# Kernel optimization log

Measured on AMD Instinct MI355X. Metric: run time of the kernel, lower is better.

Reference implementation:

```python
import jax, jax.numpy as jnp
import numpy as np

INITIAL_DELTA = 0.1
DELTA_LOW = 0.02
DELTA_HIGH = 0.1
SCAN_LEN_OFFSET = 20  # scan over num_columns - 20
EXTRA_LO, EXTRA_HI = 232, 252  # pass-through columns


def setup_inputs() -> dict:
    key = jax.random.key(0)
    x = jax.random.normal(key, (128, 1024, 252), dtype=jnp.float32)
    return {"x": x}


def _delta_modulate(x):
    # x: [B, R, C]; scan over first C-20 columns with per-(b,r) state.
    B, R, C = x.shape
    n_steps = C - SCAN_LEN_OFFSET
    xs = jnp.moveaxis(x[:, :, :n_steps], -1, 0)  # [n_steps, B, R]

    dc0 = jnp.zeros((B, R), dtype=x.dtype)
    delta0 = jnp.full((B, R), INITIAL_DELTA, dtype=x.dtype)
    tc0 = jnp.zeros((B, R), dtype=x.dtype)
    ntc0 = jnp.zeros((B, R), dtype=x.dtype)

    def step(carry, x_i):
        dc, delta, tc, ntc = carry
        up = x_i > (dc + delta)
        dn = x_i < (dc - delta)
        trig = up | dn
        tc = jnp.where(trig, tc + 1.0, 0.0)
        ntc = jnp.where(trig, 0.0, ntc + 1.0)
        delta = jnp.where(tc >= 3.0, DELTA_LOW, delta)
        delta = jnp.where(ntc >= 3.0, DELTA_HIGH, delta)
        dc = jnp.where(trig, x_i, dc)
        return (dc, delta, tc, ntc), (up, dn)

    _, (UP, DN) = jax.lax.scan(step, (dc0, delta0, tc0, ntc0), xs)
    # UP/DN: [n_steps, B, R] bool -> [B, R, n_steps]
    UP = jnp.moveaxis(UP, 0, -1)
    DN = jnp.moveaxis(DN, 0, -1)
    encoded = jnp.concatenate([UP, DN], axis=-1).astype(jnp.float32)
    extra = x[:, :, EXTRA_LO:EXTRA_HI]
    return jnp.concatenate([encoded, extra], axis=-1).astype(jnp.float32)


def reference(x) -> jnp.ndarray:
    return _delta_modulate(x)
```

## Files before the change

### kernel.cpp

```cpp
#include <hip/hip_runtime.h>

#define CC 252
#define NSTEPS 232
#define OUTC 484
#define NROWS (128 * 1024)
#define ROWS_PER_BLOCK 256

#define INITIAL_DELTA 0.1f
#define DELTA_LOW 0.02f
#define DELTA_HIGH 0.1f

#define BITS_STRIDE 17
#define EXTRA_STRIDE 21

__global__ __launch_bounds__(256) void DeltaModulator_kernel(
    const float* __restrict__ x, float* __restrict__ out)
{
    __shared__ unsigned bits_lds[ROWS_PER_BLOCK * BITS_STRIDE];
    __shared__ float    extra_lds[ROWS_PER_BLOCK * EXTRA_STRIDE];

    const int t = threadIdx.x;
    const int row0 = blockIdx.x * ROWS_PER_BLOCK;

    {
        const int row = row0 + t;
        const float* xrow = x + (size_t)row * CC;
        const float4* __restrict__ x4 = reinterpret_cast<const float4*>(xrow);

        float dc = 0.0f, delta = INITIAL_DELTA, tc = 0.0f, ntc = 0.0f;
        unsigned* __restrict__ myb = &bits_lds[t * BITS_STRIDE];

        #pragma unroll
        for (int ch = 0; ch < 7; ++ch) {
            float4 xv[8];
            #pragma unroll
            for (int k = 0; k < 8; ++k) xv[k] = x4[ch * 8 + k];
            unsigned uw = 0u, dw = 0u;
            #pragma unroll
            for (int k = 0; k < 8; ++k) {
                float xs[4] = {xv[k].x, xv[k].y, xv[k].z, xv[k].w};
                #pragma unroll
                for (int j = 0; j < 4; ++j) {
                    float xi = xs[j];
                    bool up = xi > dc + delta;
                    bool dn = xi < dc - delta;
                    bool trig = up || dn;
                    tc  = trig ? tc + 1.0f : 0.0f;
                    ntc = trig ? 0.0f : ntc + 1.0f;
                    delta = (tc  >= 3.0f) ? DELTA_LOW  : delta;
                    delta = (ntc >= 3.0f) ? DELTA_HIGH : delta;
                    dc = trig ? xi : dc;
                    uw |= (up ? 1u : 0u) << (k * 4 + j);
                    dw |= (dn ? 1u : 0u) << (k * 4 + j);
                }
            }
            myb[ch]     = uw;
            myb[8 + ch] = dw;
        }
        {
            float4 xv[2];
            #pragma unroll
            for (int k = 0; k < 2; ++k) xv[k] = x4[56 + k];
            unsigned uw = 0u, dw = 0u;
            #pragma unroll
            for (int k = 0; k < 2; ++k) {
                float xs[4] = {xv[k].x, xv[k].y, xv[k].z, xv[k].w};
                #pragma unroll
                for (int j = 0; j < 4; ++j) {
                    float xi = xs[j];
                    bool up = xi > dc + delta;
                    bool dn = xi < dc - delta;
                    bool trig = up || dn;
                    tc  = trig ? tc + 1.0f : 0.0f;
                    ntc = trig ? 0.0f : ntc + 1.0f;
                    delta = (tc  >= 3.0f) ? DELTA_LOW  : delta;
                    delta = (ntc >= 3.0f) ? DELTA_HIGH : delta;
                    dc = trig ? xi : dc;
                    uw |= (up ? 1u : 0u) << (k * 4 + j);
                    dw |= (dn ? 1u : 0u) << (k * 4 + j);
                }
            }
            myb[7]  = uw;
            myb[15] = dw;
        }
        {
            const float4* __restrict__ xe = reinterpret_cast<const float4*>(xrow + NSTEPS);
            float* __restrict__ mye = &extra_lds[t * EXTRA_STRIDE];
            #pragma unroll
            for (int i = 0; i < 5; ++i) {
                float4 v = xe[i];
                mye[i * 4 + 0] = v.x;
                mye[i * 4 + 1] = v.y;
                mye[i * 4 + 2] = v.z;
                mye[i * 4 + 3] = v.w;
            }
        }
    }

    __syncthreads();

    float4* __restrict__ o4 = reinterpret_cast<float4*>(out + (size_t)row0 * OUTC);

    int r = (t >= 242) ? 2 : ((t >= 121) ? 1 : 0);
    int f = t - r * 121;

    #pragma unroll 1
    for (int i = 0; i < 121; ++i) {
        float4 v;
        if (f < 116) {
            const int idx   = (f < 58) ? f : f - 58;
            const int wbase = (f < 58) ? 0 : 8;
            const unsigned word = bits_lds[r * BITS_STRIDE + wbase + (idx >> 3)];
            const int s = 4 * (idx & 7);
            v = make_float4((float)((word >> s) & 1u),
                            (float)((word >> (s + 1)) & 1u),
                            (float)((word >> (s + 2)) & 1u),
                            (float)((word >> (s + 3)) & 1u));
        } else {
            const float* e = &extra_lds[r * EXTRA_STRIDE + (f - 116) * 4];
            v = make_float4(e[0], e[1], e[2], e[3]);
        }
        o4[r * 121 + f] = v;

        f += 14; r += 2;
        if (f >= 121) { f -= 121; r += 1; }
    }
}

extern "C" void kernel_launch(void* const* d_in, const int* in_sizes, int n_in,
                              void* d_out, int out_size, void* d_ws, size_t ws_size,
                              hipStream_t stream) {
    const float* x = (const float*)d_in[0];
    float* out = (float*)d_out;
    const int threads = 256;
    const int blocks = NROWS / ROWS_PER_BLOCK;
    DeltaModulator_kernel<<<blocks, threads, 0, stream>>>(x, out);
}
```

Baseline: 359.2 us.

## Double-buffer row loads, shrink blocks to one wavefront, reuse loaded tail

Adds register double-buffering so the next chunk of 32 floats is loaded while the current chunk is scanned, which hides global load latency behind the serial recurrence. Blocks shrink from 256 to 64 threads (one wave) with launch bounds hinting four blocks per CU. The pass-through columns now come from the already-loaded final buffer instead of being reloaded. The output store loop is reindexed for 64 threads. The cost is more live registers for the two buffers and a larger grid of small blocks.

Result: no change. 358.6 us (-0.2%).

```diff
diff --git a/kernel.cpp b/kernel.cpp
--- a/kernel.cpp
+++ b/kernel.cpp
@@ -4,7 +4,8 @@
 #define NSTEPS 232
 #define OUTC 484
 #define NROWS (128 * 1024)
-#define ROWS_PER_BLOCK 256
+#define ROWS_PER_BLOCK 64
+#define ROW_F4_OUT 121
 
 #define INITIAL_DELTA 0.1f
 #define DELTA_LOW 0.02f
@@ -13,82 +14,81 @@
 #define BITS_STRIDE 17
 #define EXTRA_STRIDE 21
 
-__global__ __launch_bounds__(256) void DeltaModulator_kernel(
+template<int NV>
+__device__ __forceinline__ void scan_vecs(const float4* xv, unsigned& uw, unsigned& dw,
+                                          float& dc, float& delta, float& tc, float& ntc)
+{
+    uw = 0u; dw = 0u;
+    #pragma unroll
+    for (int k = 0; k < NV; ++k) {
+        float xs[4] = {xv[k].x, xv[k].y, xv[k].z, xv[k].w};
+        #pragma unroll
+        for (int j = 0; j < 4; ++j) {
+            float xi = xs[j];
+            bool up = xi > dc + delta;
+            bool dn = xi < dc - delta;
+            bool trig = up || dn;
+            tc  = trig ? tc + 1.0f : 0.0f;
+            ntc = trig ? 0.0f : ntc + 1.0f;
+            delta = (tc  >= 3.0f) ? DELTA_LOW  : delta;
+            delta = (ntc >= 3.0f) ? DELTA_HIGH : delta;
+            dc = trig ? xi : dc;
+            uw |= (up ? 1u : 0u) << (k * 4 + j);
+            dw |= (dn ? 1u : 0u) << (k * 4 + j);
+        }
+    }
+}
+
+__global__ __launch_bounds__(64, 4) void DeltaModulator_kernel(
     const float* __restrict__ x, float* __restrict__ out)
 {
     __shared__ unsigned bits_lds[ROWS_PER_BLOCK * BITS_STRIDE];
     __shared__ float    extra_lds[ROWS_PER_BLOCK * EXTRA_STRIDE];
 
-    const int t = threadIdx.x;
+    const int l = threadIdx.x;
     const int row0 = blockIdx.x * ROWS_PER_BLOCK;
+    const int row = row0 + l;
 
     {
-        const int row = row0 + t;
-        const float* xrow = x + (size_t)row * CC;
-        const float4* __restrict__ x4 = reinterpret_cast<const float4*>(xrow);
+        const float4* __restrict__ x4 =
+            reinterpret_cast<const float4*>(x + (size_t)row * CC);
 
         float dc = 0.0f, delta = INITIAL_DELTA, tc = 0.0f, ntc = 0.0f;
-        unsigned* __restrict__ myb = &bits_lds[t * BITS_STRIDE];
+        unsigned* __restrict__ myb = &bits_lds[l * BITS_STRIDE];
+
+        float4 bA[8], bB[8];
+        #pragma unroll
+        for (int k = 0; k < 8; ++k) bA[k] = x4[k];
 
         #pragma unroll
         for (int ch = 0; ch < 7; ++ch) {
-            float4 xv[8];
-            #pragma unroll
-            for (int k = 0; k < 8; ++k) xv[k] = x4[ch * 8 + k];
-            unsigned uw = 0u, dw = 0u;
-            #pragma unroll
-            for (int k = 0; k < 8; ++k) {
-                float xs[4] = {xv[k].x, xv[k].y, xv[k].z, xv[k].w};
+            const float4* cur = (ch & 1) ? bB : bA;
+            float4* nxt = (ch & 1) ? bA : bB;
+            if (ch < 6) {
                 #pragma unroll
-                for (int j = 0; j < 4; ++j) {
-                    float xi = xs[j];
-                    bool up = xi > dc + delta;
-                    bool dn = xi < dc - delta;
-                    bool trig = up || dn;
-                    tc  = trig ? tc + 1.0f : 0.0f;
-                    ntc = trig ? 0.0f : ntc + 1.0f;
-                    delta = (tc  >= 3.0f) ? DELTA_LOW  : delta;
-                    delta = (ntc >= 3.0f) ? DELTA_HIGH : delta;
-                    dc = trig ? xi : dc;
-                    uw |= (up ? 1u : 0u) << (k * 4 + j);
-                    dw |= (dn ? 1u : 0u) << (k * 4 + j);
-                }
+                for (int k = 0; k < 8; ++k) nxt[k] = x4[(ch + 1) * 8 + k];
+            } else {
+                #pragma unroll
+                for (int k = 0; k < 7; ++k) nxt[k] = x4[56 + k];
             }
+            unsigned uw, dw;
+            scan_vecs<8>(cur, uw, dw, dc, delta, tc, ntc);
             myb[ch]     = uw;
             myb[8 + ch] = dw;
         }
+
         {
-            float4 xv[2];
-            #pragma unroll
-            for (int k = 0; k < 2; ++k) xv[k] = x4[56 + k];
-            unsigned uw = 0u, dw = 0u;
-            #pragma unroll
-            for (int k = 0; k < 2; ++k) {
-                float xs[4] = {xv[k].x, xv[k].y, xv[k].z, xv[k].w};
-                #pragma unroll
-                for (int j = 0; j < 4; ++j) {
-                    float xi = xs[j];
-                    bool up = xi > dc + delta;
-                    bool dn = xi < dc - delta;
-                    bool trig = up || dn;
-                    tc  = trig ? tc + 1.0f : 0.0f;
-                    ntc = trig ? 0.0f : ntc + 1.0f;
-                    delta = (tc  >= 3.0f) ? DELTA_LOW  : delta;
-                    delta = (ntc >= 3.0f) ? DELTA_HIGH : delta;
-                    dc = trig ? xi : dc;
-                    uw |= (up ? 1u : 0u) << (k * 4 + j);
-                    dw |= (dn ? 1u : 0u) << (k * 4 + j);
-                }
-            }
+            unsigned uw, dw;
+            scan_vecs<2>(bB, uw, dw, dc, delta, tc, ntc);
             myb[7]  = uw;
             myb[15] = dw;
         }
+
         {
-            const float4* __restrict__ xe = reinterpret_cast<const float4*>(xrow + NSTEPS);
-            float* __restrict__ mye = &extra_lds[t * EXTRA_STRIDE];
+            float* __restrict__ mye = &extra_lds[l * EXTRA_STRIDE];
             #pragma unroll
             for (int i = 0; i < 5; ++i) {
-                float4 v = xe[i];
+                float4 v = bB[2 + i];
                 mye[i * 4 + 0] = v.x;
                 mye[i * 4 + 1] = v.y;
                 mye[i * 4 + 2] = v.z;
@@ -101,28 +101,28 @@
 
     float4* __restrict__ o4 = reinterpret_cast<float4*>(out + (size_t)row0 * OUTC);
 
-    int r = (t >= 242) ? 2 : ((t >= 121) ? 1 : 0);
-    int f = t - r * 121;
+    int r = 0;
+    int f = l;
 
     #pragma unroll 1
     for (int i = 0; i < 121; ++i) {
-        float4 v;
+        float4 w;
         if (f < 116) {
             const int idx   = (f < 58) ? f : f - 58;
             const int wbase = (f < 58) ? 0 : 8;
             const unsigned word = bits_lds[r * BITS_STRIDE + wbase + (idx >> 3)];
             const int s = 4 * (idx & 7);
-            v = make_float4((float)((word >> s) & 1u),
+            w = make_float4((float)((word >> s) & 1u),
                             (float)((word >> (s + 1)) & 1u),
                             (float)((word >> (s + 2)) & 1u),
                             (float)((word >> (s + 3)) & 1u));
         } else {
             const float* e = &extra_lds[r * EXTRA_STRIDE + (f - 116) * 4];
-            v = make_float4(e[0], e[1], e[2], e[3]);
+            w = make_float4(e[0], e[1], e[2], e[3]);
         }
-        o4[r * 121 + f] = v;
+        o4[r * ROW_F4_OUT + f] = w;
 
-        f += 14; r += 2;
+        f += 64;
         if (f >= 121) { f -= 121; r += 1; }
     }
 }
@@ -132,7 +132,7 @@
                               hipStream_t stream) {
     const float* x = (const float*)d_in[0];
     float* out = (float*)d_out;
-    const int threads = 256;
+    const int threads = 64;
     const int blocks = NROWS / ROWS_PER_BLOCK;
     DeltaModulator_kernel<<<blocks, threads, 0, stream>>>(x, out);
 }
```
